# Kernel tuning notes

Measured on AMD Instinct MI355X. Metric: run time of the kernel, lower is better.

Reference implementation:

```python
import jax, jax.numpy as jnp
import numpy as np

BS, S, WIDTH, MODES = 2, 512, 64, 16
P = S * (S - 1) // 2
IU, JU = np.triu_indices(S, 1)  # upper-triangle (i<j) index constants
COLL_COEF = 0.9  # training=True path


def spectral_conv(x, w):
    # x: (bs, c_in, n), w: (c_in, c_out, modes, 2)
    n = x.shape[-1]
    xf = jnp.fft.rfft(x, axis=2, norm='ortho')  # (bs, c_in, n//2+1) complex
    wm = w[..., 0] + 1j * w[..., 1]
    out_m = jnp.einsum('bix,iox->box', xf[:, :, :MODES], wm)
    pad = jnp.zeros((x.shape[0], w.shape[1], n // 2 + 1 - MODES), dtype=out_m.dtype)
    return jnp.fft.irfft(jnp.concatenate([out_m, pad], axis=2), n=n, axis=2, norm='ortho')


def dsmc(x, a, rvec):
    # x, a: (bs, c, n); rvec: (bs, c, P) unit vectors along c.  dt=1, v = a*dt.
    bs, c, n = x.shape
    v = a
    x_r = jnp.linalg.norm(x[:, :, :, None] - x[:, :, None, :], axis=1)  # (bs, n, n)
    v_r = jnp.linalg.norm(v[:, :, :, None] - v[:, :, None, :], axis=1)
    v_cm = (v[:, :, :, None] + v[:, :, None, :]) * 0.5  # (bs, c, n, n)
    x_cm = (x[:, :, :, None] + x[:, :, None, :]) * 0.5
    u_x = jnp.exp(-x_r)
    v_r_max = jnp.max(v_r, axis=(1, 2), keepdims=True)  # (bs,1,1)
    mask = v_r / v_r_max * u_x
    cm = mask > (1.0 - COLL_COEF)  # collision mask (bs, n, n)
    # antisymmetric projection of v_r upper triangle onto random unit vectors
    proj = v_r[:, IU, JU][:, None, :] * rvec  # (bs, c, P)
    vrl = (jnp.zeros((bs, c, n, n), x.dtype)
           .at[:, :, IU, JU].set(proj)
           .at[:, :, JU, IU].set(-proj))
    delta_v = v_cm + vrl - v[:, :, :, None]
    cmf = cm.astype(x.dtype)
    v_new = v + jnp.sum(delta_v * cmf[:, None], axis=2)  # sum over partners i
    cmf = cmf + jnp.eye(n, dtype=x.dtype)[None]  # add self
    x_new = jnp.sum(x_cm * cmf[:, None], axis=2) / jnp.sum(cmf, axis=2)[:, None, :]
    x_new = x_new + v_new  # x = x + v*dt
    return x_new, v_new


def setup_inputs() -> dict:
    key = jax.random.key(0)
    ks = jax.random.split(key, 12)
    x = jax.random.normal(ks[0], (BS, S, 2), jnp.float32)
    v = jax.random.normal(ks[1], (BS, WIDTH, S), jnp.float32)
    vecs = jax.random.normal(ks[2], (4, BS, WIDTH, P), jnp.float32)
    vecs = vecs / jnp.linalg.norm(vecs, axis=2, keepdims=True)  # unit vectors over chnl
    fc0_w = jax.random.normal(ks[3], (2, WIDTH), jnp.float32) * 0.5
    fc0_b = jax.random.normal(ks[4], (WIDTH,), jnp.float32) * 0.1
    scale = 1.0 / (WIDTH * WIDTH)
    spec_w = jax.random.uniform(ks[5], (4, WIDTH, WIDTH, MODES, 2), jnp.float32) * scale
    conv_w = jax.random.normal(ks[6], (4, WIDTH, WIDTH), jnp.float32) * (WIDTH ** -0.5)
    conv_b = jax.random.normal(ks[7], (4, WIDTH), jnp.float32) * 0.05
    fc1_w = jax.random.normal(ks[8], (WIDTH, 128), jnp.float32) * (WIDTH ** -0.5)
    fc1_b = jnp.zeros((128,), jnp.float32)
    fc2_w = jax.random.normal(ks[9], (128, 1), jnp.float32) * (128 ** -0.5)
    fc2_b = jnp.zeros((1,), jnp.float32)
    return {"x": x, "v": v, "vecs": vecs, "fc0_w": fc0_w, "fc0_b": fc0_b,
            "spec_w": spec_w, "conv_w": conv_w, "conv_b": conv_b,
            "fc1_w": fc1_w, "fc1_b": fc1_b, "fc2_w": fc2_w, "fc2_b": fc2_b}


def reference(x, v, vecs, fc0_w, fc0_b, spec_w, conv_w, conv_b, fc1_w, fc1_b, fc2_w, fc2_b):
    # NOTE: v is overwritten by a*dt inside KINET_DSMC2 in the original; kept for signature fidelity.
    h = x @ fc0_w + fc0_b          # (bs, s, width)
    h = jnp.transpose(h, (0, 2, 1))  # (bs, width, s)
    for i in range(4):
        a = spectral_conv(h, spec_w[i])
        p = jnp.einsum('oi,bin->bon', conv_w[i], h) + conv_b[i][None, :, None]
        h, vv = dsmc(p, a, vecs[i])
        if i < 3:
            h = jax.nn.relu(h)
    h = jnp.transpose(h, (0, 2, 1))  # (bs, s, width)
    h = jax.nn.relu(h @ fc1_w + fc1_b)
    return h @ fc2_w + fc2_b  # (bs, s, 1)
```

## Files before the change

### kernel.cpp

```cpp
#include <hip/hip_runtime.h>
#include <math.h>

#define S 512
#define W 64
#define MODES 16
#define PAIRS 130816
#define INV_SQRT_N 0.04419417382415922f
#define TWO_PI_OVER_N 0.012271846303085130f

__global__ __launch_bounds__(256) void k_fc0(const float* __restrict__ x,
                                             const float* __restrict__ w,
                                             const float* __restrict__ bias,
                                             float* __restrict__ h) {
    int b = blockIdx.x >> 6, c = blockIdx.x & 63;
    int tid = threadIdx.x;
    float w0 = w[c], w1 = w[64 + c], bb = bias[c];
    for (int t = tid; t < S; t += 256) {
        float x0 = x[(b * S + t) * 2];
        float x1 = x[(b * S + t) * 2 + 1];
        h[(b * W + c) * S + t] = x0 * w0 + x1 * w1 + bb;
    }
}

__global__ __launch_bounds__(256) void k_fft(const float* __restrict__ h,
                                             float* __restrict__ Xf) {
    int b = blockIdx.x >> 6, ch = blockIdx.x & 63;
    int tid = threadIdx.x;
    const float* hp = h + (b * W + ch) * S;
    float v0 = hp[tid], v1 = hp[tid + 256];
    float re[MODES], im[MODES];
#pragma unroll
    for (int m = 0; m < MODES; ++m) {
        float sn, cs;
        sincosf(TWO_PI_OVER_N * (float)(m * tid), &sn, &cs);
        float a = (m & 1) ? (v0 - v1) : (v0 + v1);
        re[m] = a * cs;
        im[m] = -a * sn;
    }
    __shared__ float part[4][32];
    int lane = tid & 63, wv = tid >> 6;
#pragma unroll
    for (int m = 0; m < MODES; ++m) {
        float r = re[m], ii = im[m];
        for (int off = 32; off; off >>= 1) {
            r += __shfl_down(r, off);
            ii += __shfl_down(ii, off);
        }
        if (lane == 0) { part[wv][2 * m] = r; part[wv][2 * m + 1] = ii; }
    }
    __syncthreads();
    if (tid < 32) {
        float s = part[0][tid] + part[1][tid] + part[2][tid] + part[3][tid];
        Xf[(b * W + ch) * 32 + tid] = s * INV_SQRT_N;
    }
}

__global__ __launch_bounds__(256) void k_mix(const float* __restrict__ Xf,
                                             const float* __restrict__ specw,
                                             float* __restrict__ Y, int l) {
    int b = blockIdx.x >> 6, o = blockIdx.x & 63;
    int tid = threadIdx.x, m = tid & 15, ip = tid >> 4;
    __shared__ float Xs[2048];
    for (int idx = tid; idx < 2048; idx += 256) Xs[idx] = Xf[b * 2048 + idx];
    __syncthreads();
    float ar = 0.f, ai = 0.f;
#pragma unroll
    for (int q = 0; q < 4; ++q) {
        int i = ip * 4 + q;
        const float* wp = specw + (size_t)(((l * W + i) * W + o) * MODES + m) * 2;
        float wr = wp[0], wi = wp[1];
        float xr = Xs[i * 32 + 2 * m], xi = Xs[i * 32 + 2 * m + 1];
        ar += xr * wr - xi * wi;
        ai += xr * wi + xi * wr;
    }
    __shared__ float redr[16][17], redi[16][17];
    redr[ip][m] = ar; redi[ip][m] = ai;
    __syncthreads();
    if (tid < 16) {
        float sr = 0.f, si = 0.f;
        for (int p = 0; p < 16; ++p) { sr += redr[p][tid]; si += redi[p][tid]; }
        Y[(b * W + o) * 32 + 2 * tid] = sr;
        Y[(b * W + o) * 32 + 2 * tid + 1] = si;
    }
}

__global__ __launch_bounds__(256) void k_ac(const float* __restrict__ Y,
                                            const float* __restrict__ h,
                                            const float* __restrict__ convw,
                                            const float* __restrict__ convb,
                                            float* __restrict__ aT,
                                            float* __restrict__ pT,
                                            unsigned* __restrict__ vmax, int l) {
    int blk = blockIdx.x;
    int b = blk >> 7, t0 = (blk & 127) * 4;
    int tid = threadIdx.x;
    int o = tid & 63, tg = tid >> 6;
    if (blk == 0 && tid < 2) vmax[tid] = 0u;
    __shared__ float hs[64 * 5];
    if (tid < 256) {
        int r = tid >> 2, t = tid & 3;
        hs[r * 5 + t] = h[(b * W + r) * S + t0 + t];
    }
    float yr[MODES], yi[MODES];
    const float4* yp = (const float4*)(Y + b * 2048 + o * 32);
#pragma unroll
    for (int q = 0; q < 8; ++q) {
        float4 y4 = yp[q];
        yr[2 * q] = y4.x; yi[2 * q] = y4.y;
        yr[2 * q + 1] = y4.z; yi[2 * q + 1] = y4.w;
    }
    int t = t0 + tg;
    float acc = yr[0];
#pragma unroll
    for (int m = 1; m < MODES; ++m) {
        float sn, cs;
        sincosf(TWO_PI_OVER_N * (float)(m * t), &sn, &cs);
        acc += 2.0f * (yr[m] * cs - yi[m] * sn);
    }
    aT[((size_t)b * S + t) * W + o] = acc * INV_SQRT_N;
    __syncthreads();
    float pacc = convb[l * W + o];
    const float4* wp = (const float4*)(convw + l * 4096 + o * 64);
#pragma unroll
    for (int i4 = 0; i4 < 16; ++i4) {
        float4 w4 = wp[i4];
        pacc = fmaf(w4.x, hs[(4 * i4 + 0) * 5 + tg], pacc);
        pacc = fmaf(w4.y, hs[(4 * i4 + 1) * 5 + tg], pacc);
        pacc = fmaf(w4.z, hs[(4 * i4 + 2) * 5 + tg], pacc);
        pacc = fmaf(w4.w, hs[(4 * i4 + 3) * 5 + tg], pacc);
    }
    pT[((size_t)b * S + t) * W + o] = pacc;
}

__global__ __launch_bounds__(256) void k_pair(const float* __restrict__ pT,
                                              const float* __restrict__ aT,
                                              float* __restrict__ vr,
                                              float* __restrict__ uxm,
                                              unsigned* __restrict__ vmax) {
    int blk = blockIdx.x;
    int b = blk >> 8;
    int rest = blk & 255;
    int i0 = (rest & 15) * 32, j0 = (rest >> 4) * 32;
    int tid = threadIdx.x;
    int tx = tid & 15, ty = tid >> 4;
    __shared__ float Pi[64 * 33], Pj[64 * 33], Vi[64 * 33], Vj[64 * 33];
    for (int idx = tid; idx < 2048; idx += 256) {
        int k = idx >> 6, c = idx & 63;
        Pi[c * 33 + k] = pT[(b * S + i0 + k) * W + c];
        Pj[c * 33 + k] = pT[(b * S + j0 + k) * W + c];
        Vi[c * 33 + k] = aT[(b * S + i0 + k) * W + c];
        Vj[c * 33 + k] = aT[(b * S + j0 + k) * W + c];
    }
    __syncthreads();
    float ax[2][2] = {{0.f, 0.f}, {0.f, 0.f}};
    float av[2][2] = {{0.f, 0.f}, {0.f, 0.f}};
    for (int c = 0; c < W; ++c) {
        float pi0 = Pi[c * 33 + 2 * tx], pi1 = Pi[c * 33 + 2 * tx + 1];
        float pj0 = Pj[c * 33 + 2 * ty], pj1 = Pj[c * 33 + 2 * ty + 1];
        float vi0 = Vi[c * 33 + 2 * tx], vi1 = Vi[c * 33 + 2 * tx + 1];
        float vj0 = Vj[c * 33 + 2 * ty], vj1 = Vj[c * 33 + 2 * ty + 1];
        float d;
        d = pi0 - pj0; ax[0][0] = fmaf(d, d, ax[0][0]);
        d = pi1 - pj0; ax[1][0] = fmaf(d, d, ax[1][0]);
        d = pi0 - pj1; ax[0][1] = fmaf(d, d, ax[0][1]);
        d = pi1 - pj1; ax[1][1] = fmaf(d, d, ax[1][1]);
        d = vi0 - vj0; av[0][0] = fmaf(d, d, av[0][0]);
        d = vi1 - vj0; av[1][0] = fmaf(d, d, av[1][0]);
        d = vi0 - vj1; av[0][1] = fmaf(d, d, av[0][1]);
        d = vi1 - vj1; av[1][1] = fmaf(d, d, av[1][1]);
    }
    float mx = 0.f;
#pragma unroll
    for (int jj = 0; jj < 2; ++jj) {
#pragma unroll
        for (int ii = 0; ii < 2; ++ii) {
            int i = i0 + 2 * tx + ii, j = j0 + 2 * ty + jj;
            float xr = sqrtf(ax[ii][jj]);
            float vv = sqrtf(av[ii][jj]);
            vr[((size_t)b * S + j) * S + i] = vv;
            uxm[((size_t)b * S + j) * S + i] = expf(-xr);
            mx = fmaxf(mx, vv);
        }
    }
    for (int off = 32; off; off >>= 1) mx = fmaxf(mx, __shfl_xor(mx, off));
    if ((tid & 63) == 0) atomicMax(&vmax[b], __float_as_uint(mx));
}

__global__ __launch_bounds__(256) void k_mask(const float* __restrict__ vr,
                                              const float* __restrict__ uxm,
                                              const unsigned* __restrict__ vmaxu,
                                              const float* __restrict__ aT,
                                              const float* __restrict__ pT,
                                              float* __restrict__ wpair,
                                              float* __restrict__ sv,
                                              float* __restrict__ sx,
                                              int* __restrict__ Acnt,
                                              float* __restrict__ Tg) {
    int b = blockIdx.x >> 9, j = blockIdx.x & 511;
    int tid = threadIdx.x, lane = tid & 63, wv = tid >> 6;
    __shared__ float wrow[S];
    __shared__ float SV[4][64], SX[4][64];
    __shared__ int cnt4[4];
    const float* vrp = vr + ((size_t)b * S + j) * S;
    const float* uxp = uxm + ((size_t)b * S + j) * S;
    float vmax = __uint_as_float(vmaxu[b]);
    int mycnt = 0;
    for (int i = tid; i < S; i += 256) {
        float v = vrp[i], u = uxp[i];
        bool act = (v / vmax) * u > 0.1f;
        wrow[i] = act ? v : 0.f;
        mycnt += act ? 1 : 0;
    }
    for (int o = 32; o; o >>= 1) mycnt += __shfl_down(mycnt, o);
    if (lane == 0) cnt4[wv] = mycnt;
    __syncthreads();
    int A = cnt4[0] + cnt4[1] + cnt4[2] + cnt4[3];
    if (tid == 0) Acnt[b * S + j] = A;
    if (tid < 64) Tg[((size_t)b * S + j) * W + tid] = 0.f;
    size_t tri = (size_t)j * 511 - (((size_t)j * (j - 1)) >> 1);
    for (int i = j + 1 + tid; i < S; i += 256)
        wpair[(size_t)b * PAIRS + tri + (i - j - 1)] = wrow[i];
    float svp = 0.f, sxp = 0.f;
    const float* aTb = aT + (size_t)b * S * W;
    const float* pTb = pT + (size_t)b * S * W;
    for (int k = 0; k < 128; ++k) {
        int i = wv * 128 + k;
        if (wrow[i] != 0.f) {
            svp += aTb[i * W + lane];
            sxp += pTb[i * W + lane];
        }
    }
    SV[wv][lane] = svp; SX[wv][lane] = sxp;
    __syncthreads();
    if (tid < 64) {
        sv[((size_t)b * S + j) * W + tid] = SV[0][tid] + SV[1][tid] + SV[2][tid] + SV[3][tid];
        sx[((size_t)b * S + j) * W + tid] = SX[0][tid] + SX[1][tid] + SX[2][tid] + SX[3][tid];
    }
}

__global__ __launch_bounds__(256) void k_proj2(const float* __restrict__ wpair,
                                               const float* __restrict__ vecs,
                                               float* __restrict__ Tg, int l) {
    int tile = blockIdx.x, cg = blockIdx.y, b = blockIdx.z;
    int ti = 0, rem = tile;
    while (rem >= 8 - ti) { rem -= 8 - ti; ++ti; }
    int tj = ti + rem;
    int i0 = ti * 64, j0 = tj * 64;
    int tid = threadIdx.x, lane = tid & 63, wv = tid >> 6;
    __shared__ float Tjs[4][64][9];
    __shared__ float Tis[64][9];
    for (int k2 = tid; k2 < 4 * 64 * 9; k2 += 256) ((float*)Tjs)[k2] = 0.f;
    for (int k2 = tid; k2 < 64 * 9; k2 += 256) ((float*)Tis)[k2] = 0.f;
    __syncthreads();
    const float* wb = wpair + (size_t)b * PAIRS;
    const float* Rb = vecs + (size_t)((l * 2 + b) * W + cg * 8) * PAIRS;
    float accj[8] = {0.f, 0.f, 0.f, 0.f, 0.f, 0.f, 0.f, 0.f};
    int gj = j0 + lane;
    for (int s = 0; s < 16; ++s) {
        int li = wv + 4 * s;
        int gi = i0 + li;
        int pbase = gi * 511 - ((gi * (gi - 1)) >> 1) + (j0 - gi - 1);
        bool valid = gj > gi;
        int idx = valid ? (pbase + lane) : 0;
        float w = wb[idx];
        if (!valid) w = 0.f;
        if (__ballot(w != 0.f) == 0ull) continue;
        float part[8];
#pragma unroll
        for (int cc = 0; cc < 8; ++cc) {
            float r = Rb[(size_t)cc * PAIRS + idx];
            float p = w * r;
            accj[cc] += p;
            part[cc] = p;
        }
#pragma unroll
        for (int cc = 0; cc < 8; ++cc) {
            float p = part[cc];
            for (int o = 32; o; o >>= 1) p += __shfl_xor(p, o);
            if (lane == 0) Tis[li][cc] = p;
        }
    }
#pragma unroll
    for (int cc = 0; cc < 8; ++cc) Tjs[wv][lane][cc] = accj[cc];
    __syncthreads();
    for (int k2 = tid; k2 < 512; k2 += 256) {
        int r = k2 >> 3, cc = k2 & 7;
        float sj = Tjs[0][r][cc] + Tjs[1][r][cc] + Tjs[2][r][cc] + Tjs[3][r][cc];
        if (sj != 0.f)
            atomicAdd(&Tg[((size_t)b * S + j0 + r) * W + cg * 8 + cc], sj);
        float si = Tis[r][cc];
        if (si != 0.f)
            atomicAdd(&Tg[((size_t)b * S + i0 + r) * W + cg * 8 + cc], -si);
    }
}

__global__ __launch_bounds__(256) void k_fin(const float* __restrict__ aT,
                                             const float* __restrict__ pT,
                                             const float* __restrict__ sv,
                                             const float* __restrict__ sx,
                                             const int* __restrict__ Acnt,
                                             const float* __restrict__ Tg,
                                             float* __restrict__ h_std,
                                             const float* __restrict__ fc1w,
                                             const float* __restrict__ fc1b,
                                             const float* __restrict__ fc2w,
                                             const float* __restrict__ fc2b,
                                             float* __restrict__ out,
                                             int do_relu, int do_head) {
    int wv = threadIdx.x >> 6;
    int g = blockIdx.x * 4 + wv;
    int b = g >> 9, j = g & 511;
    int c = threadIdx.x & 63;
    size_t row = ((size_t)b * S + j) * W;
    float A = (float)Acnt[b * S + j];
    float vj = aT[row + c], xj = pT[row + c];
    float vnew = vj + 0.5f * (A * vj - sv[row + c]) + Tg[row + c];
    float accx = 0.5f * (A * xj + sx[row + c]);
    float xnew = (xj + accx) / (A + 1.0f) + vnew;
    if (do_relu) xnew = fmaxf(xnew, 0.0f);
    if (!do_head) {
        h_std[((size_t)b * W + c) * S + j] = xnew;
        return;
    }
    __shared__ float hsh[4][64];
    hsh[wv][c] = xnew;
    __syncthreads();
    float a0 = fc1b[c], a1 = fc1b[c + 64];
    for (int cc = 0; cc < W; ++cc) {
        float hv = hsh[wv][cc];
        a0 = fmaf(hv, fc1w[cc * 128 + c], a0);
        a1 = fmaf(hv, fc1w[cc * 128 + c + 64], a1);
    }
    a0 = fmaxf(a0, 0.f); a1 = fmaxf(a1, 0.f);
    float p = a0 * fc2w[c] + a1 * fc2w[c + 64];
    for (int off = 32; off; off >>= 1) p += __shfl_down(p, off);
    if (c == 0) out[b * S + j] = p + fc2b[0];
}

extern "C" void kernel_launch(void* const* d_in, const int* in_sizes, int n_in,
                              void* d_out, int out_size, void* d_ws, size_t ws_size,
                              hipStream_t stream) {
    const float* x = (const float*)d_in[0];
    const float* vecs = (const float*)d_in[2];
    const float* fc0w = (const float*)d_in[3];
    const float* fc0b = (const float*)d_in[4];
    const float* specw = (const float*)d_in[5];
    const float* convw = (const float*)d_in[6];
    const float* convb = (const float*)d_in[7];
    const float* fc1w = (const float*)d_in[8];
    const float* fc1b = (const float*)d_in[9];
    const float* fc2w = (const float*)d_in[10];
    const float* fc2b = (const float*)d_in[11];
    float* out = (float*)d_out;

    char* ws = (char*)d_ws;
    unsigned* vmax = (unsigned*)ws;
    float* h_std = (float*)(ws + 256);
    float* hT = h_std + 65536;
    float* aT = hT + 65536;
    float* pT = aT + 65536;
    float* Xf = pT + 65536;
    float* Yb = Xf + 4096;
    float* vrbuf = Yb + 4096;
    float* uxbuf = vrbuf + 524288;
    float* Tg = uxbuf + 524288;
    float* svb = Tg + 65536;
    float* sxb = svb + 65536;
    int* Acnt = (int*)(sxb + 65536);
    float* wpair = (float*)(Acnt + 1024);
    (void)hT;

    k_fc0<<<128, 256, 0, stream>>>(x, fc0w, fc0b, h_std);
    for (int l = 0; l < 4; ++l) {
        k_fft<<<128, 256, 0, stream>>>(h_std, Xf);
        k_mix<<<128, 256, 0, stream>>>(Xf, specw, Yb, l);
        k_ac<<<256, 256, 0, stream>>>(Yb, h_std, convw, convb, aT, pT, vmax, l);
        k_pair<<<512, 256, 0, stream>>>(pT, aT, vrbuf, uxbuf, vmax);
        k_mask<<<1024, 256, 0, stream>>>(vrbuf, uxbuf, vmax, aT, pT,
                                         wpair, svb, sxb, Acnt, Tg);
        k_proj2<<<dim3(36, 8, 2), 256, 0, stream>>>(wpair, vecs, Tg, l);
        k_fin<<<256, 256, 0, stream>>>(aT, pT, svb, sxb, Acnt, Tg,
                                       h_std, fc1w, fc1b, fc2w, fc2b, out,
                                       (l < 3) ? 1 : 0, (l == 3) ? 1 : 0);
    }
}
```

Before: 733.2 us.

## Fuse mask, projection and finalize into one per-row kernel; fold fc0 into FFT

Merges k_mask, k_proj2 and k_fin into a single per-row kernel, k_mpf. It computes the collision mask row, the partner sums and the antisymmetric random-vector projection, then applies the update and head directly. This removes the wpair, Tg, sv, sx and Acnt intermediates, the atomics and two launches per layer. fc0 is recomputed inside k_fft and k_ac for the first layer, dropping the separate k_fc0 launch. The trade-off is that the projection now gathers vecs with a strided triangular index per active pair (one channel per lane), so reads are uncoalesced across lanes, replacing the previous tiled, coalesced access. The vmax atomic is also reduced to one atomic per block.

```diff
diff --git a/kernel.cpp b/kernel.cpp
--- a/kernel.cpp
+++ b/kernel.cpp
@@ -8,26 +8,23 @@
 #define INV_SQRT_N 0.04419417382415922f
 #define TWO_PI_OVER_N 0.012271846303085130f
 
-__global__ __launch_bounds__(256) void k_fc0(const float* __restrict__ x,
-                                             const float* __restrict__ w,
-                                             const float* __restrict__ bias,
-                                             float* __restrict__ h) {
-    int b = blockIdx.x >> 6, c = blockIdx.x & 63;
-    int tid = threadIdx.x;
-    float w0 = w[c], w1 = w[64 + c], bb = bias[c];
-    for (int t = tid; t < S; t += 256) {
-        float x0 = x[(b * S + t) * 2];
-        float x1 = x[(b * S + t) * 2 + 1];
-        h[(b * W + c) * S + t] = x0 * w0 + x1 * w1 + bb;
-    }
-}
-
 __global__ __launch_bounds__(256) void k_fft(const float* __restrict__ h,
-                                             float* __restrict__ Xf) {
+                                             const float* __restrict__ x,
+                                             const float* __restrict__ fc0w,
+                                             const float* __restrict__ fc0b,
+                                             float* __restrict__ Xf, int first) {
     int b = blockIdx.x >> 6, ch = blockIdx.x & 63;
     int tid = threadIdx.x;
-    const float* hp = h + (b * W + ch) * S;
-    float v0 = hp[tid], v1 = hp[tid + 256];
+    float v0, v1;
+    if (first) {
+        float w0 = fc0w[ch], w1 = fc0w[64 + ch], bb = fc0b[ch];
+        const float* xb = x + (size_t)b * S * 2;
+        v0 = xb[2 * tid] * w0 + xb[2 * tid + 1] * w1 + bb;
+        v1 = xb[2 * (tid + 256)] * w0 + xb[2 * (tid + 256) + 1] * w1 + bb;
+    } else {
+        const float* hp = h + (b * W + ch) * S;
+        v0 = hp[tid]; v1 = hp[tid + 256];
+    }
     float re[MODES], im[MODES];
 #pragma unroll
     for (int m = 0; m < MODES; ++m) {
@@ -86,20 +83,29 @@
 
 __global__ __launch_bounds__(256) void k_ac(const float* __restrict__ Y,
                                             const float* __restrict__ h,
+                                            const float* __restrict__ x,
+                                            const float* __restrict__ fc0w,
+                                            const float* __restrict__ fc0b,
                                             const float* __restrict__ convw,
                                             const float* __restrict__ convb,
                                             float* __restrict__ aT,
                                             float* __restrict__ pT,
-                                            unsigned* __restrict__ vmax, int l) {
+                                            unsigned* __restrict__ vmax,
+                                            int l, int first) {
     int blk = blockIdx.x;
     int b = blk >> 7, t0 = (blk & 127) * 4;
     int tid = threadIdx.x;
     int o = tid & 63, tg = tid >> 6;
     if (blk == 0 && tid < 2) vmax[tid] = 0u;
     __shared__ float hs[64 * 5];
-    if (tid < 256) {
+    {
         int r = tid >> 2, t = tid & 3;
-        hs[r * 5 + t] = h[(b * W + r) * S + t0 + t];
+        if (first) {
+            const float* xb = x + ((size_t)b * S + t0 + t) * 2;
+            hs[r * 5 + t] = xb[0] * fc0w[r] + xb[1] * fc0w[64 + r] + fc0b[r];
+        } else {
+            hs[r * 5 + t] = h[(b * W + r) * S + t0 + t];
+        }
     }
     float yr[MODES], yi[MODES];
     const float4* yp = (const float4*)(Y + b * 2048 + o * 32);
@@ -182,27 +188,37 @@
             mx = fmaxf(mx, vv);
         }
     }
+    __shared__ float mxs[4];
     for (int off = 32; off; off >>= 1) mx = fmaxf(mx, __shfl_xor(mx, off));
-    if ((tid & 63) == 0) atomicMax(&vmax[b], __float_as_uint(mx));
-}
-
-__global__ __launch_bounds__(256) void k_mask(const float* __restrict__ vr,
-                                              const float* __restrict__ uxm,
-                                              const unsigned* __restrict__ vmaxu,
-                                              const float* __restrict__ aT,
-                                              const float* __restrict__ pT,
-                                              float* __restrict__ wpair,
-                                              float* __restrict__ sv,
-                                              float* __restrict__ sx,
-                                              int* __restrict__ Acnt,
-                                              float* __restrict__ Tg) {
-    int b = blockIdx.x >> 9, j = blockIdx.x & 511;
+    if ((tid & 63) == 0) mxs[tid >> 6] = mx;
+    __syncthreads();
+    if (tid == 0) {
+        float m = fmaxf(fmaxf(mxs[0], mxs[1]), fmaxf(mxs[2], mxs[3]));
+        atomicMax(&vmax[b], __float_as_uint(m));
+    }
+}
+
+__global__ __launch_bounds__(256) void k_mpf(const float* __restrict__ vr,
+                                             const float* __restrict__ uxm,
+                                             const unsigned* __restrict__ vmaxu,
+                                             const float* __restrict__ aT,
+                                             const float* __restrict__ pT,
+                                             const float* __restrict__ vecs,
+                                             float* __restrict__ h_std,
+                                             const float* __restrict__ fc1w,
+                                             const float* __restrict__ fc1b,
+                                             const float* __restrict__ fc2w,
+                                             const float* __restrict__ fc2b,
+                                             float* __restrict__ out,
+                                             int l, int do_relu, int do_head) {
+    int b = blockIdx.x >> 9, q = blockIdx.x & 511;
     int tid = threadIdx.x, lane = tid & 63, wv = tid >> 6;
     __shared__ float wrow[S];
-    __shared__ float SV[4][64], SX[4][64];
+    __shared__ float SV[4][64], SX[4][64], TP[4][64];
+    __shared__ float hrow[64];
     __shared__ int cnt4[4];
-    const float* vrp = vr + ((size_t)b * S + j) * S;
-    const float* uxp = uxm + ((size_t)b * S + j) * S;
+    const float* vrp = vr + ((size_t)b * S + q) * S;
+    const float* uxp = uxm + ((size_t)b * S + q) * S;
     float vmax = __uint_as_float(vmaxu[b]);
     int mycnt = 0;
     for (int i = tid; i < S; i += 256) {
@@ -214,127 +230,53 @@
     for (int o = 32; o; o >>= 1) mycnt += __shfl_down(mycnt, o);
     if (lane == 0) cnt4[wv] = mycnt;
     __syncthreads();
-    int A = cnt4[0] + cnt4[1] + cnt4[2] + cnt4[3];
-    if (tid == 0) Acnt[b * S + j] = A;
-    if (tid < 64) Tg[((size_t)b * S + j) * W + tid] = 0.f;
-    size_t tri = (size_t)j * 511 - (((size_t)j * (j - 1)) >> 1);
-    for (int i = j + 1 + tid; i < S; i += 256)
-        wpair[(size_t)b * PAIRS + tri + (i - j - 1)] = wrow[i];
-    float svp = 0.f, sxp = 0.f;
+    float A = (float)(cnt4[0] + cnt4[1] + cnt4[2] + cnt4[3]);
+    float svp = 0.f, sxp = 0.f, tp = 0.f;
     const float* aTb = aT + (size_t)b * S * W;
     const float* pTb = pT + (size_t)b * S * W;
+    const float* Rb = vecs + (size_t)((l * 2 + b) * W + lane) * PAIRS;
+    int triq = q * 511 - ((q * (q - 1)) >> 1);
     for (int k = 0; k < 128; ++k) {
-        int i = wv * 128 + k;
-        if (wrow[i] != 0.f) {
-            svp += aTb[i * W + lane];
-            sxp += pTb[i * W + lane];
-        }
-    }
-    SV[wv][lane] = svp; SX[wv][lane] = sxp;
-    __syncthreads();
-    if (tid < 64) {
-        sv[((size_t)b * S + j) * W + tid] = SV[0][tid] + SV[1][tid] + SV[2][tid] + SV[3][tid];
-        sx[((size_t)b * S + j) * W + tid] = SX[0][tid] + SX[1][tid] + SX[2][tid] + SX[3][tid];
-    }
-}
-
-__global__ __launch_bounds__(256) void k_proj2(const float* __restrict__ wpair,
-                                               const float* __restrict__ vecs,
-                                               float* __restrict__ Tg, int l) {
-    int tile = blockIdx.x, cg = blockIdx.y, b = blockIdx.z;
-    int ti = 0, rem = tile;
-    while (rem >= 8 - ti) { rem -= 8 - ti; ++ti; }
-    int tj = ti + rem;
-    int i0 = ti * 64, j0 = tj * 64;
-    int tid = threadIdx.x, lane = tid & 63, wv = tid >> 6;
-    __shared__ float Tjs[4][64][9];
-    __shared__ float Tis[64][9];
-    for (int k2 = tid; k2 < 4 * 64 * 9; k2 += 256) ((float*)Tjs)[k2] = 0.f;
-    for (int k2 = tid; k2 < 64 * 9; k2 += 256) ((float*)Tis)[k2] = 0.f;
-    __syncthreads();
-    const float* wb = wpair + (size_t)b * PAIRS;
-    const float* Rb = vecs + (size_t)((l * 2 + b) * W + cg * 8) * PAIRS;
-    float accj[8] = {0.f, 0.f, 0.f, 0.f, 0.f, 0.f, 0.f, 0.f};
-    int gj = j0 + lane;
-    for (int s = 0; s < 16; ++s) {
-        int li = wv + 4 * s;
-        int gi = i0 + li;
-        int pbase = gi * 511 - ((gi * (gi - 1)) >> 1) + (j0 - gi - 1);
-        bool valid = gj > gi;
-        int idx = valid ? (pbase + lane) : 0;
-        float w = wb[idx];
-        if (!valid) w = 0.f;
-        if (__ballot(w != 0.f) == 0ull) continue;
-        float part[8];
-#pragma unroll
-        for (int cc = 0; cc < 8; ++cc) {
-            float r = Rb[(size_t)cc * PAIRS + idx];
-            float p = w * r;
-            accj[cc] += p;
-            part[cc] = p;
-        }
-#pragma unroll
-        for (int cc = 0; cc < 8; ++cc) {
-            float p = part[cc];
-            for (int o = 32; o; o >>= 1) p += __shfl_xor(p, o);
-            if (lane == 0) Tis[li][cc] = p;
-        }
-    }
-#pragma unroll
-    for (int cc = 0; cc < 8; ++cc) Tjs[wv][lane][cc] = accj[cc];
-    __syncthreads();
-    for (int k2 = tid; k2 < 512; k2 += 256) {
-        int r = k2 >> 3, cc = k2 & 7;
-        float sj = Tjs[0][r][cc] + Tjs[1][r][cc] + Tjs[2][r][cc] + Tjs[3][r][cc];
-        if (sj != 0.f)
-            atomicAdd(&Tg[((size_t)b * S + j0 + r) * W + cg * 8 + cc], sj);
-        float si = Tis[r][cc];
-        if (si != 0.f)
-            atomicAdd(&Tg[((size_t)b * S + i0 + r) * W + cg * 8 + cc], -si);
-    }
-}
-
-__global__ __launch_bounds__(256) void k_fin(const float* __restrict__ aT,
-                                             const float* __restrict__ pT,
-                                             const float* __restrict__ sv,
-                                             const float* __restrict__ sx,
-                                             const int* __restrict__ Acnt,
-                                             const float* __restrict__ Tg,
-                                             float* __restrict__ h_std,
-                                             const float* __restrict__ fc1w,
-                                             const float* __restrict__ fc1b,
-                                             const float* __restrict__ fc2w,
-                                             const float* __restrict__ fc2b,
-                                             float* __restrict__ out,
-                                             int do_relu, int do_head) {
-    int wv = threadIdx.x >> 6;
-    int g = blockIdx.x * 4 + wv;
-    int b = g >> 9, j = g & 511;
-    int c = threadIdx.x & 63;
-    size_t row = ((size_t)b * S + j) * W;
-    float A = (float)Acnt[b * S + j];
-    float vj = aT[row + c], xj = pT[row + c];
-    float vnew = vj + 0.5f * (A * vj - sv[row + c]) + Tg[row + c];
-    float accx = 0.5f * (A * xj + sx[row + c]);
-    float xnew = (xj + accx) / (A + 1.0f) + vnew;
-    if (do_relu) xnew = fmaxf(xnew, 0.0f);
-    if (!do_head) {
-        h_std[((size_t)b * W + c) * S + j] = xnew;
-        return;
-    }
-    __shared__ float hsh[4][64];
-    hsh[wv][c] = xnew;
-    __syncthreads();
-    float a0 = fc1b[c], a1 = fc1b[c + 64];
-    for (int cc = 0; cc < W; ++cc) {
-        float hv = hsh[wv][cc];
-        a0 = fmaf(hv, fc1w[cc * 128 + c], a0);
-        a1 = fmaf(hv, fc1w[cc * 128 + c + 64], a1);
-    }
-    a0 = fmaxf(a0, 0.f); a1 = fmaxf(a1, 0.f);
-    float p = a0 * fc2w[c] + a1 * fc2w[c + 64];
-    for (int off = 32; off; off >>= 1) p += __shfl_down(p, off);
-    if (c == 0) out[b * S + j] = p + fc2b[0];
+        int p = wv * 128 + k;
+        float w = wrow[p];
+        if (w != 0.f) {
+            svp += aTb[p * W + lane];
+            sxp += pTb[p * W + lane];
+            int idx; float sgn;
+            if (p < q) { idx = p * 511 - ((p * (p - 1)) >> 1) + (q - p - 1); sgn = 1.f; }
+            else       { idx = triq + (p - q - 1); sgn = -1.f; }
+            tp = fmaf(sgn * w, Rb[idx], tp);
+        }
+    }
+    SV[wv][lane] = svp; SX[wv][lane] = sxp; TP[wv][lane] = tp;
+    __syncthreads();
+    if (wv == 0) {
+        float sv = SV[0][lane] + SV[1][lane] + SV[2][lane] + SV[3][lane];
+        float sx = SX[0][lane] + SX[1][lane] + SX[2][lane] + SX[3][lane];
+        float T  = TP[0][lane] + TP[1][lane] + TP[2][lane] + TP[3][lane];
+        float vj = aTb[q * W + lane], xj = pTb[q * W + lane];
+        float vnew = vj + 0.5f * (A * vj - sv) + T;
+        float accx = 0.5f * (A * xj + sx);
+        float xnew = (xj + accx) / (A + 1.0f) + vnew;
+        if (do_relu) xnew = fmaxf(xnew, 0.0f);
+        if (!do_head) h_std[((size_t)b * W + lane) * S + q] = xnew;
+        else hrow[lane] = xnew;
+    }
+    if (do_head) {
+        __syncthreads();
+        if (wv == 0) {
+            float a0 = fc1b[lane], a1 = fc1b[lane + 64];
+            for (int cc = 0; cc < W; ++cc) {
+                float hv = hrow[cc];
+                a0 = fmaf(hv, fc1w[cc * 128 + lane], a0);
+                a1 = fmaf(hv, fc1w[cc * 128 + lane + 64], a1);
+            }
+            a0 = fmaxf(a0, 0.f); a1 = fmaxf(a1, 0.f);
+            float p = a0 * fc2w[lane] + a1 * fc2w[lane + 64];
+            for (int off = 32; off; off >>= 1) p += __shfl_down(p, off);
+            if (lane == 0) out[b * S + q] = p + fc2b[0];
+        }
+    }
 }
 
 extern "C" void kernel_launch(void* const* d_in, const int* in_sizes, int n_in,
@@ -356,31 +298,22 @@
     char* ws = (char*)d_ws;
     unsigned* vmax = (unsigned*)ws;
     float* h_std = (float*)(ws + 256);
-    float* hT = h_std + 65536;
-    float* aT = hT + 65536;
+    float* aT = h_std + 65536;
     float* pT = aT + 65536;
     float* Xf = pT + 65536;
     float* Yb = Xf + 4096;
     float* vrbuf = Yb + 4096;
     float* uxbuf = vrbuf + 524288;
-    float* Tg = uxbuf + 524288;
-    float* svb = Tg + 65536;
-    float* sxb = svb + 65536;
-    int* Acnt = (int*)(sxb + 65536);
-    float* wpair = (float*)(Acnt + 1024);
-    (void)hT;
-
-    k_fc0<<<128, 256, 0, stream>>>(x, fc0w, fc0b, h_std);
+
     for (int l = 0; l < 4; ++l) {
-        k_fft<<<128, 256, 0, stream>>>(h_std, Xf);
+        int first = (l == 0) ? 1 : 0;
+        k_fft<<<128, 256, 0, stream>>>(h_std, x, fc0w, fc0b, Xf, first);
         k_mix<<<128, 256, 0, stream>>>(Xf, specw, Yb, l);
-        k_ac<<<256, 256, 0, stream>>>(Yb, h_std, convw, convb, aT, pT, vmax, l);
+        k_ac<<<256, 256, 0, stream>>>(Yb, h_std, x, fc0w, fc0b, convw, convb,
+                                      aT, pT, vmax, l, first);
         k_pair<<<512, 256, 0, stream>>>(pT, aT, vrbuf, uxbuf, vmax);
-        k_mask<<<1024, 256, 0, stream>>>(vrbuf, uxbuf, vmax, aT, pT,
-                                         wpair, svb, sxb, Acnt, Tg);
-        k_proj2<<<dim3(36, 8, 2), 256, 0, stream>>>(wpair, vecs, Tg, l);
-        k_fin<<<256, 256, 0, stream>>>(aT, pT, svb, sxb, Acnt, Tg,
-                                       h_std, fc1w, fc1b, fc2w, fc2b, out,
-                                       (l < 3) ? 1 : 0, (l == 3) ? 1 : 0);
-    }
-}
+        k_mpf<<<1024, 256, 0, stream>>>(vrbuf, uxbuf, vmax, aT, pT, vecs,
+                                        h_std, fc1w, fc1b, fc2w, fc2b, out,
+                                        l, (l < 3) ? 1 : 0, (l == 3) ? 1 : 0);
+    }
+}
```

Result: faster. 655.9 us (-10.5%).
